# Kernel tuning notes

Measured on AMD Instinct MI355X. Metric: run time of the kernel, lower is better.

The kernel has to match this reference:

```python
import jax, jax.numpy as jnp
import numpy as np

B, S, D, H = 1, 2048, 2048, 32
HD = D // H
SCALE = float(HD) ** -0.5


def _rope(x, cos, sin):
    # x: (b, s, h, hd); interleaved-pair RoPE as in executorch apply_rotary_emb
    xr, xi = x[..., 0::2], x[..., 1::2]
    c = cos[None, :, None, :]
    s = sin[None, :, None, :]
    out = jnp.stack([xr * c - xi * s, xr * s + xi * c], axis=-1)
    return out.reshape(x.shape)


def setup_inputs() -> dict:
    key = jax.random.key(0)
    ks = jax.random.split(key, 8)
    hidden_states = jax.random.normal(ks[0], (B, S, D), jnp.float32)
    pos = jnp.arange(S, dtype=jnp.float32)
    inv = 1.0 / (10000.0 ** (jnp.arange(0, HD, 2, dtype=jnp.float32) / HD))
    ang = pos[:, None] * inv[None, :]  # (S, HD//2)
    freqs_cos = jnp.cos(ang)
    freqs_sin = jnp.sin(ang)
    causal = jnp.tril(jnp.ones((S, S), dtype=bool))
    attention_mask = jnp.where(causal, 0.0, -1e9).astype(jnp.float32)[None, None]
    k_cache = jax.random.normal(ks[1], (B, S, H, HD), jnp.float32)
    v_cache = jax.random.normal(ks[2], (B, S, H, HD), jnp.float32)
    k_mask = jnp.ones((B, S, 1, 1), jnp.float32)
    v_mask = jnp.ones((B, S, 1, 1), jnp.float32)
    # weights stored as (in, out); math-equivalent to torch Linear(out,in) @ W.T
    wq = jax.random.normal(ks[3], (D, D), jnp.float32) * 0.02
    wk = jax.random.normal(ks[4], (D, D), jnp.float32) * 0.02
    wv = jax.random.normal(ks[5], (D, D), jnp.float32) * 0.02
    wo = jax.random.normal(ks[6], (D, D), jnp.float32) * 0.02
    return {"hidden_states": hidden_states, "freqs_cos": freqs_cos,
            "freqs_sin": freqs_sin, "attention_mask": attention_mask,
            "k_cache": k_cache, "v_cache": v_cache,
            "k_mask": k_mask, "v_mask": v_mask,
            "wq": wq, "wk": wk, "wv": wv, "wo": wo}


def reference(hidden_states, freqs_cos, freqs_sin, attention_mask,
              k_cache, v_cache, k_mask, v_mask, wq, wk, wv, wo):
    b, s, _ = hidden_states.shape
    q = (hidden_states @ wq).reshape(b, s, H, HD)
    k = (hidden_states @ wk).reshape(b, s, H, HD)
    v = (hidden_states @ wv).reshape(b, s, H, HD)
    q = _rope(q, freqs_cos, freqs_sin)
    k = _rope(k, freqs_cos, freqs_sin)
    # mask-blend KV cache update
    k = k_cache * (1.0 - k_mask) + k * k_mask  # (b, S, H, HD)
    v = v_cache * (1.0 - v_mask) + v * v_mask
    qt = q.transpose(0, 2, 1, 3)  # (b, H, s, HD)
    kt = k.transpose(0, 2, 1, 3)
    vt = v.transpose(0, 2, 1, 3)
    attn = jnp.einsum('bhqd,bhkd->bhqk', qt, kt) * SCALE + attention_mask
    attn = jax.nn.softmax(attn, axis=-1)
    y = jnp.einsum('bhqk,bhkd->bhqd', attn, vt)  # (b, H, s, HD)
    # torch: y.transpose(0,1).contiguous().view(b, s, dim); valid since b == 1
    y = jnp.swapaxes(y, 0, 1).reshape(b, s, D)
    y = y @ wo
    return (y, k, v)
```

## Files before the change

kernel.cpp:

```cpp
#include <hip/hip_runtime.h>
#include <hip/hip_bf16.h>
#include <stdint.h>

typedef __bf16 bf16;
typedef __attribute__((ext_vector_type(8))) __bf16 bf16x8;
typedef __attribute__((ext_vector_type(4))) float f32x4;

#define SEQ 2048
#define DIM 2048
#define NHEAD 32
#define HD 64
#define SCALE_L2E 0.18033688011112042f

__device__ __forceinline__ void gload16(void* lds, const void* g) {
  __builtin_amdgcn_global_load_lds(
      (const __attribute__((address_space(1))) unsigned int*)g,
      (__attribute__((address_space(3))) unsigned int*)lds, 16, 0, 0);
}

__device__ __forceinline__ f32x4 mfma16(bf16x8 a, bf16x8 b, f32x4 c) {
  return __builtin_amdgcn_mfma_f32_16x16x32_bf16(a, b, c, 0, 0, 0);
}

__global__ __launch_bounds__(256) void prep(
    const float* __restrict__ hs, bf16* __restrict__ hsb,
    const float* __restrict__ w0, const float* __restrict__ w1,
    const float* __restrict__ w2, const float* __restrict__ w3,
    bf16* __restrict__ t0, bf16* __restrict__ t1,
    bf16* __restrict__ t2, bf16* __restrict__ t3) {
  int t = threadIdx.x;
  if (blockIdx.z == 4) {
    size_t i = ((size_t)(blockIdx.y * 32 + blockIdx.x) * 256 + t) * 16;
#pragma unroll
    for (int half = 0; half < 2; ++half) {
      f32x4 a = *(const f32x4*)(hs + i + half * 8);
      f32x4 b = *(const f32x4*)(hs + i + half * 8 + 4);
      bf16x8 o;
#pragma unroll
      for (int j = 0; j < 4; ++j) { o[j] = (bf16)a[j]; o[j + 4] = (bf16)b[j]; }
      *(bf16x8*)(hsb + i + half * 8) = o;
    }
    return;
  }
  const float* wsrc[4] = {w0, w1, w2, w3};
  bf16* wdst[4] = {t0, t1, t2, t3};
  const float* w = wsrc[blockIdx.z];
  bf16* wT = wdst[blockIdx.z];
  __shared__ alignas(16) bf16 tile[64][72];
  int n0 = blockIdx.x * 64, k0 = blockIdx.y * 64;
#pragma unroll
  for (int i = 0; i < 4; ++i) {
    int r = (t >> 4) + 16 * i;
    int c = (t & 15) * 4;
    f32x4 v = *(const f32x4*)(w + (size_t)(k0 + r) * DIM + n0 + c);
#pragma unroll
    for (int j = 0; j < 4; ++j) tile[r][c + j] = (bf16)v[j];
  }
  __syncthreads();
#pragma unroll
  for (int i = 0; i < 2; ++i) {
    int n = (t >> 3) + 32 * i;
    int kb = (t & 7) * 8;
    bf16x8 o;
#pragma unroll
    for (int j = 0; j < 8; ++j) o[j] = tile[kb + j][n];
    *(bf16x8*)(wT + (size_t)(n0 + n) * DIM + k0 + kb) = o;
  }
}

template <typename OutT>
__global__ __launch_bounds__(256) void gemm128(
    const bf16* __restrict__ A,
    const bf16* __restrict__ B0, const bf16* __restrict__ B1, const bf16* __restrict__ B2,
    OutT* __restrict__ C0, OutT* __restrict__ C1, OutT* __restrict__ C2,
    int M, int N, int K) {
  const bf16* Bt; OutT* C;
  if (blockIdx.z == 0)      { Bt = B0; C = C0; }
  else if (blockIdx.z == 1) { Bt = B1; C = C1; }
  else                      { Bt = B2; C = C2; }
  __shared__ alignas(16) bf16 As[128][64];
  __shared__ alignas(16) bf16 Bs[128][64];
  int tid = threadIdx.x, lane = tid & 63, w = tid >> 6;
  int wr = w >> 1, wc = w & 1;
  size_t mBase = (size_t)blockIdx.y * 128, nBase = (size_t)blockIdx.x * 128;
  f32x4 acc[4][4] = {};
  int r0 = tid >> 3, sl = tid & 7;
  int lr = lane & 15, hi = lane >> 4, sw = lr & 7;
  for (int kt = 0; kt < K; kt += 64) {
#pragma unroll
    for (int i = 0; i < 4; ++i) {
      int row = r0 + 32 * i;
      int kc = sl ^ (row & 7);
      gload16(&As[row][sl * 8], A + (mBase + row) * K + kt + kc * 8);
      gload16(&Bs[row][sl * 8], Bt + (nBase + row) * K + kt + kc * 8);
    }
    __syncthreads();
#pragma unroll
    for (int kk = 0; kk < 2; ++kk) {
      int cb = kk * 4 + hi;
      bf16x8 a[4], b[4];
#pragma unroll
      for (int m = 0; m < 4; ++m)
        a[m] = *(const bf16x8*)&As[wr * 64 + m * 16 + lr][(cb ^ sw) * 8];
#pragma unroll
      for (int n = 0; n < 4; ++n)
        b[n] = *(const bf16x8*)&Bs[wc * 64 + n * 16 + lr][(cb ^ sw) * 8];
#pragma unroll
      for (int m = 0; m < 4; ++m)
#pragma unroll
        for (int n = 0; n < 4; ++n)
          acc[m][n] = mfma16(a[m], b[n], acc[m][n]);
    }
    __syncthreads();
  }
#pragma unroll
  for (int m = 0; m < 4; ++m)
#pragma unroll
    for (int n = 0; n < 4; ++n)
#pragma unroll
      for (int j = 0; j < 4; ++j) {
        size_t row = mBase + wr * 64 + m * 16 + hi * 4 + j;
        size_t col = nBase + wc * 64 + n * 16 + lr;
        C[row * N + col] = (OutT)acc[m][n][j];
      }
}

__global__ __launch_bounds__(512) void gemm_out(
    const bf16* __restrict__ A, const bf16* __restrict__ Bt,
    float* __restrict__ Y) {
  const int K = DIM, N = DIM;
  __shared__ alignas(16) bf16 As[2][128][64];
  __shared__ alignas(16) bf16 Bs[2][128][64];
  __shared__ alignas(16) float red[128][132];
  int tid = threadIdx.x;
  int grp = tid >> 8;
  int gt = tid & 255;
  int lane = gt & 63, w = gt >> 6;
  int wr = w >> 1, wc = w & 1;
  size_t mBase = (size_t)blockIdx.y * 128, nBase = (size_t)blockIdx.x * 128;
  f32x4 acc[4][4] = {};
  int r0 = gt >> 3, sl = gt & 7;
  int lr = lane & 15, hi = lane >> 4, sw = lr & 7;
  int kbeg = grp * (K / 2);
  for (int kt = kbeg; kt < kbeg + K / 2; kt += 64) {
#pragma unroll
    for (int i = 0; i < 4; ++i) {
      int row = r0 + 32 * i;
      int kc = sl ^ (row & 7);
      gload16(&As[grp][row][sl * 8], A + (mBase + row) * K + kt + kc * 8);
      gload16(&Bs[grp][row][sl * 8], Bt + (nBase + row) * K + kt + kc * 8);
    }
    __syncthreads();
#pragma unroll
    for (int kk = 0; kk < 2; ++kk) {
      int cb = kk * 4 + hi;
      bf16x8 a[4], b[4];
#pragma unroll
      for (int m = 0; m < 4; ++m)
        a[m] = *(const bf16x8*)&As[grp][wr * 64 + m * 16 + lr][(cb ^ sw) * 8];
#pragma unroll
      for (int n = 0; n < 4; ++n)
        b[n] = *(const bf16x8*)&Bs[grp][wc * 64 + n * 16 + lr][(cb ^ sw) * 8];
#pragma unroll
      for (int m = 0; m < 4; ++m)
#pragma unroll
        for (int n = 0; n < 4; ++n)
          acc[m][n] = mfma16(a[m], b[n], acc[m][n]);
    }
    __syncthreads();
  }
  if (grp == 1) {
#pragma unroll
    for (int m = 0; m < 4; ++m)
#pragma unroll
      for (int n = 0; n < 4; ++n)
#pragma unroll
        for (int j = 0; j < 4; ++j)
          red[wr * 64 + m * 16 + hi * 4 + j][wc * 64 + n * 16 + lr] = acc[m][n][j];
  }
  __syncthreads();
  if (grp == 0) {
#pragma unroll
    for (int m = 0; m < 4; ++m)
#pragma unroll
      for (int n = 0; n < 4; ++n)
#pragma unroll
        for (int j = 0; j < 4; ++j) {
          int row = wr * 64 + m * 16 + hi * 4 + j;
          int col = wc * 64 + n * 16 + lr;
          Y[(mBase + row) * N + nBase + col] = acc[m][n][j] + red[row][col];
        }
  }
}

__global__ __launch_bounds__(256) void qkvprep(
    const bf16* __restrict__ qraw, const bf16* __restrict__ kraw,
    const bf16* __restrict__ vraw,
    const float* __restrict__ fc, const float* __restrict__ fs,
    const float* __restrict__ kcache, const float* __restrict__ kmask,
    const float* __restrict__ vcache, const float* __restrict__ vmask,
    float* __restrict__ kout, float* __restrict__ vout,
    bf16* __restrict__ qb, bf16* __restrict__ kb, bf16* __restrict__ vtb) {
  __shared__ alignas(16) bf16 tile[64][72];
  int bid = blockIdx.x;
  if (bid < SEQ) {
    int s = bid;
    int c0 = threadIdx.x * 8;
    int h = c0 >> 6, d0 = c0 & 63;
    float km = kmask[s], omk = 1.0f - km;
    size_t src = (size_t)s * DIM + c0;
    f32x4 cc = *(const f32x4*)(fc + s * 32 + (d0 >> 1));
    f32x4 ss = *(const f32x4*)(fs + s * 32 + (d0 >> 1));
    bf16x8 qv = *(const bf16x8*)(qraw + src);
    bf16x8 kv = *(const bf16x8*)(kraw + src);
    float kcf[8];
    *(f32x4*)(kcf) = *(const f32x4*)(kcache + src);
    *(f32x4*)(kcf + 4) = *(const f32x4*)(kcache + src + 4);
    bf16x8 qo, ko;
    float kof[8];
#pragma unroll
    for (int i = 0; i < 4; ++i) {
      float c = cc[i], sn = ss[i];
      float qr = (float)qv[2 * i], qi = (float)qv[2 * i + 1];
      qo[2 * i]     = (bf16)(qr * c - qi * sn);
      qo[2 * i + 1] = (bf16)(qr * sn + qi * c);
      float kr = (float)kv[2 * i], ki = (float)kv[2 * i + 1];
      float b0 = kcf[2 * i] * omk + (kr * c - ki * sn) * km;
      float b1 = kcf[2 * i + 1] * omk + (kr * sn + ki * c) * km;
      kof[2 * i] = b0; kof[2 * i + 1] = b1;
      ko[2 * i] = (bf16)b0; ko[2 * i + 1] = (bf16)b1;
    }
    *(f32x4*)(kout + src) = *(f32x4*)kof;
    *(f32x4*)(kout + src + 4) = *(f32x4*)(kof + 4);
    size_t dsth = ((size_t)h * SEQ + s) * HD + d0;
    *(bf16x8*)(qb + dsth) = qo;
    *(bf16x8*)(kb + dsth) = ko;
    return;
  }
  int vb = bid - SEQ;
  int h = vb >> 5;
  int s0 = (vb & 31) * 64;
  int t = threadIdx.x;
#pragma unroll
  for (int i = 0; i < 4; ++i) {
    int r = (t >> 4) + 16 * i;
    int c = (t & 15) * 4;
    int s = s0 + r;
    float vm = vmask[s], om = 1.0f - vm;
    size_t src = (size_t)s * DIM + h * 64 + c;
    f32x4 vc = *(const f32x4*)(vcache + src);
    f32x4 o;
#pragma unroll
    for (int j = 0; j < 4; ++j) {
      float val = vc[j] * om + (float)vraw[src + j] * vm;
      o[j] = val;
      tile[r][c + j] = (bf16)val;
    }
    *(f32x4*)(vout + src) = o;
  }
  __syncthreads();
#pragma unroll
  for (int i = 0; i < 2; ++i) {
    int hd = (t >> 3) + 32 * i;
    int cb = (t & 7) * 8;
    bf16x8 o;
#pragma unroll
    for (int j = 0; j < 8; ++j) o[j] = tile[cb + j][hd];
    *(bf16x8*)(vtb + (size_t)h * HD * SEQ + (size_t)hd * SEQ + s0 + cb) = o;
  }
}

__global__ __launch_bounds__(512) void attn_fwd(
    const bf16* __restrict__ qb, const bf16* __restrict__ kb,
    const bf16* __restrict__ vtb, bf16* __restrict__ ob) {
  int orig = blockIdx.x;
  int wg = (orig & 7) * 32 + (orig >> 3);
  int h = wg >> 3;
  int qp = wg & 7;
  int qtA = qp, qtB = 15 - qp;
  int ntA = qtA + 1;
  const int NT = 17;
  __shared__ alignas(16) bf16 Ks[2][128][64];
  __shared__ alignas(16) bf16 Vs[2][64][128];
  __shared__ alignas(16) bf16 Ps[8][16][128];
  int tid = threadIdx.x, lane = tid & 63, w = tid >> 6;
  const bf16* qh = qb + (size_t)h * SEQ * HD;
  const bf16* kh = kb + (size_t)h * SEQ * HD;
  const bf16* vh = vtb + (size_t)h * HD * SEQ;
  int lr = lane & 15, hi = lane >> 4, sw = lr & 7;
  int qrowA = qtA * 128 + w * 16 + lr;
  int qrowB = qtB * 128 + w * 16 + lr;
  bf16x8 qfA[2], qfB[2];
#pragma unroll
  for (int kk = 0; kk < 2; ++kk) {
    qfA[kk] = *(const bf16x8*)(qh + (size_t)qrowA * HD + kk * 32 + hi * 8);
    qfB[kk] = *(const bf16x8*)(qh + (size_t)qrowB * HD + kk * 32 + hi * 8);
  }
  f32x4 otA[4] = {}, otB[4] = {};
  float mA = -3e38f, lA = 0.f, mB = -3e38f, lB = 0.f;
  char* PsW = (char*)&Ps[w][0][0];

  auto STAGE = [&](int kv0, int b) {
    int kr0 = tid >> 3, ksl = tid & 7;
#pragma unroll
    for (int i = 0; i < 2; ++i) {
      int row = kr0 + 64 * i;
      int kc = ksl ^ (row & 7);
      gload16(&Ks[b][row][ksl * 8], kh + (size_t)(kv0 + row) * HD + kc * 8);
    }
    int vr0 = tid >> 4, vsl = tid & 15;
#pragma unroll
    for (int i = 0; i < 2; ++i) {
      int row = vr0 + 32 * i;
      int vc = vsl ^ (row & 7);
      gload16(&Vs[b][row][vsl * 8], vh + (size_t)row * SEQ + kv0 + vc * 8);
    }
  };

  auto BODY = [&](int buf, int kv0, bf16x8 (&qf)[2], f32x4 (&ot)[4],
                  float& mrun, float& lrun, int qrow, bool last) {
    f32x4 st[8] = {};
    __builtin_amdgcn_s_setprio(1);
#pragma unroll
    for (int kk = 0; kk < 2; ++kk) {
      int cb = kk * 4 + hi;
#pragma unroll
      for (int n = 0; n < 8; ++n) {
        bf16x8 kf = *(const bf16x8*)&Ks[buf][n * 16 + lr][(cb ^ sw) * 8];
        st[n] = mfma16(kf, qf[kk], st[n]);
      }
    }
    __builtin_amdgcn_s_setprio(0);
    if (last) {
#pragma unroll
      for (int n = 0; n < 8; ++n)
#pragma unroll
        for (int j = 0; j < 4; ++j) {
          int key = kv0 + n * 16 + hi * 4 + j;
          st[n][j] = (key <= qrow) ? st[n][j] * SCALE_L2E : -1e30f;
        }
    } else {
#pragma unroll
      for (int n = 0; n < 8; ++n)
#pragma unroll
        for (int j = 0; j < 4; ++j) st[n][j] *= SCALE_L2E;
    }
    float tm[8];
#pragma unroll
    for (int n = 0; n < 8; ++n)
      tm[n] = fmaxf(fmaxf(st[n][0], st[n][1]), fmaxf(st[n][2], st[n][3]));
    float t01 = fmaxf(tm[0], tm[1]), t23 = fmaxf(tm[2], tm[3]);
    float t45 = fmaxf(tm[4], tm[5]), t67 = fmaxf(tm[6], tm[7]);
    float tmax = fmaxf(fmaxf(t01, t23), fmaxf(t45, t67));
    tmax = fmaxf(tmax, __shfl_xor(tmax, 16));
    tmax = fmaxf(tmax, __shfl_xor(tmax, 32));
    if (!__all(tmax <= mrun + 8.f)) {
      float mnew = fmaxf(mrun, tmax);
      float alpha = exp2f(mrun - mnew);
      mrun = mnew;
      lrun *= alpha;
#pragma unroll
      for (int nd = 0; nd < 4; ++nd)
#pragma unroll
        for (int j = 0; j < 4; ++j) ot[nd][j] *= alpha;
    }
    float ps[8];
#pragma unroll
    for (int n = 0; n < 8; ++n) {
      float p0 = exp2f(st[n][0] - mrun), p1 = exp2f(st[n][1] - mrun);
      float p2 = exp2f(st[n][2] - mrun), p3 = exp2f(st[n][3] - mrun);
      st[n][0] = p0; st[n][1] = p1; st[n][2] = p2; st[n][3] = p3;
      ps[n] = (p0 + p1) + (p2 + p3);
    }
    float psum = ((ps[0] + ps[1]) + (ps[2] + ps[3])) +
                 ((ps[4] + ps[5]) + (ps[6] + ps[7]));
    psum += __shfl_xor(psum, 16);
    psum += __shfl_xor(psum, 32);
    lrun += psum;
#pragma unroll
    for (int n = 0; n < 8; ++n) {
      union { bf16 b[4]; uint2 u; } pk;
#pragma unroll
      for (int j = 0; j < 4; ++j) pk.b[j] = (bf16)st[n][j];
      int keyc = n * 2 + (hi >> 1);
      *(uint2*)(PsW + lr * 256 + ((keyc ^ sw) * 16) + (hi & 1) * 8) = pk.u;
    }
    __builtin_amdgcn_s_setprio(1);
#pragma unroll
    for (int kk = 0; kk < 4; ++kk) {
      int cb = kk * 4 + hi;
      bf16x8 pf = *(const bf16x8*)(PsW + lr * 256 + ((cb ^ sw) * 16));
#pragma unroll
      for (int nd = 0; nd < 4; ++nd) {
        bf16x8 vf = *(const bf16x8*)&Vs[buf][nd * 16 + lr][(cb ^ sw) * 8];
        ot[nd] = mfma16(vf, pf, ot[nd]);
      }
    }
    __builtin_amdgcn_s_setprio(0);
  };

  auto STORE = [&](f32x4 (&ot)[4], float lrun, int qrow) {
    float rinv = 1.0f / lrun;
    bf16* orow = ob + ((size_t)h * SEQ + qrow) * HD;
#pragma unroll
    for (int nd = 0; nd < 4; ++nd) {
      union { bf16 b[4]; uint2 u; } o;
#pragma unroll
      for (int j = 0; j < 4; ++j) o.b[j] = (bf16)(ot[nd][j] * rinv);
      *(uint2*)(orow + nd * 16 + hi * 4) = o.u;
    }
  };

  STAGE(0, 0);
  int buf = 0;
  for (int t = 0; t < NT; ++t) {
    __syncthreads();
    if (t + 1 < NT) {
      int tn = t + 1;
      int kvn = (tn < ntA ? tn : tn - ntA) * 128;
      STAGE(kvn, buf ^ 1);
    }
    if (t < ntA) {
      int kv0 = t * 128;
      BODY(buf, kv0, qfA, otA, mA, lA, qrowA, t == ntA - 1);
      if (t == ntA - 1) STORE(otA, lA, qrowA);
    } else {
      int kv0 = (t - ntA) * 128;
      BODY(buf, kv0, qfB, otB, mB, lB, qrowB, t == NT - 1);
    }
    buf ^= 1;
  }
  STORE(otB, lB, qrowB);
}

extern "C" void kernel_launch(void* const* d_in, const int* in_sizes, int n_in,
                              void* d_out, int out_size, void* d_ws, size_t ws_size,
                              hipStream_t stream) {
  const float* hs     = (const float*)d_in[0];
  const float* fc     = (const float*)d_in[1];
  const float* fs     = (const float*)d_in[2];
  const float* kcache = (const float*)d_in[4];
  const float* vcache = (const float*)d_in[5];
  const float* kmask  = (const float*)d_in[6];
  const float* vmask  = (const float*)d_in[7];
  const float* wq     = (const float*)d_in[8];
  const float* wk     = (const float*)d_in[9];
  const float* wv     = (const float*)d_in[10];
  const float* wo     = (const float*)d_in[11];

  float* y    = (float*)d_out;
  float* kout = y + (size_t)SEQ * DIM;
  float* vout = y + 2 * (size_t)SEQ * DIM;

  char* ws = (char*)d_ws;
  const size_t MB8 = (size_t)SEQ * DIM * sizeof(bf16);
  bf16* wqT  = (bf16*)(ws + 0 * MB8);
  bf16* wkT  = (bf16*)(ws + 1 * MB8);
  bf16* wvT  = (bf16*)(ws + 2 * MB8);
  bf16* woT  = (bf16*)(ws + 3 * MB8);
  bf16* hsb  = (bf16*)(ws + 4 * MB8);
  bf16* qraw = (bf16*)(ws + 5 * MB8);
  bf16* kraw = (bf16*)(ws + 6 * MB8);
  bf16* vraw = (bf16*)(ws + 7 * MB8);
  bf16* qb   = (bf16*)(ws + 8 * MB8);
  bf16* kb   = (bf16*)(ws + 9 * MB8);
  bf16* vtb  = (bf16*)(ws + 10 * MB8);
  bf16* ob   = hsb;

  prep<<<dim3(32, 32, 5), dim3(256), 0, stream>>>(
      hs, hsb, wq, wk, wv, wo, wqT, wkT, wvT, woT);
  gemm128<bf16><<<dim3(16, 16, 3), dim3(256), 0, stream>>>(
      hsb, wqT, wkT, wvT, qraw, kraw, vraw, SEQ, DIM, DIM);
  qkvprep<<<dim3(SEQ + 1024), dim3(256), 0, stream>>>(
      qraw, kraw, vraw, fc, fs, kcache, kmask, vcache, vmask,
      kout, vout, qb, kb, vtb);
  attn_fwd<<<dim3(256), dim3(512), 0, stream>>>(qb, kb, vtb, ob);
  gemm_out<<<dim3(16, 16), dim3(512), 0, stream>>>(ob, woT, y);
}
```

Baseline: 188.0 us.

## Replace QKV projection GEMM with 256x256 tiled, double-buffered 8-wave pipelined kernel

Replaces the single-buffered 128x128 QKV GEMM with a 256x256 tile kernel using 512 threads (8 waves), double-buffered LDS split into two k-halves, and prefetch of upcoming k-slices interleaved with MFMA phases under barriers and setprio. It also remaps blocks with a swizzled tile order and uses a new LDS XOR swizzle. The aims are to overlap global loads with compute, raise arithmetic intensity per tile, and cut sync stalls. The cost is higher register pressure (8x4 accumulators) and fewer blocks (192) spread across the CUs.

```diff
diff --git a/kernel.cpp b/kernel.cpp
--- a/kernel.cpp
+++ b/kernel.cpp
@@ -68,60 +68,93 @@
   }
 }
 
-template <typename OutT>
-__global__ __launch_bounds__(256) void gemm128(
+__global__ __launch_bounds__(512, 2) void gemm8p(
     const bf16* __restrict__ A,
     const bf16* __restrict__ B0, const bf16* __restrict__ B1, const bf16* __restrict__ B2,
-    OutT* __restrict__ C0, OutT* __restrict__ C1, OutT* __restrict__ C2,
-    int M, int N, int K) {
-  const bf16* Bt; OutT* C;
+    bf16* __restrict__ C0, bf16* __restrict__ C1, bf16* __restrict__ C2) {
+  const int K = DIM, N = DIM;
+  const bf16* Bt; bf16* C;
   if (blockIdx.z == 0)      { Bt = B0; C = C0; }
   else if (blockIdx.z == 1) { Bt = B1; C = C1; }
   else                      { Bt = B2; C = C2; }
-  __shared__ alignas(16) bf16 As[128][64];
-  __shared__ alignas(16) bf16 Bs[128][64];
-  int tid = threadIdx.x, lane = tid & 63, w = tid >> 6;
-  int wr = w >> 1, wc = w & 1;
-  size_t mBase = (size_t)blockIdx.y * 128, nBase = (size_t)blockIdx.x * 128;
-  f32x4 acc[4][4] = {};
-  int r0 = tid >> 3, sl = tid & 7;
-  int lr = lane & 15, hi = lane >> 4, sw = lr & 7;
-  for (int kt = 0; kt < K; kt += 64) {
-#pragma unroll
-    for (int i = 0; i < 4; ++i) {
-      int row = r0 + 32 * i;
-      int kc = sl ^ (row & 7);
-      gload16(&As[row][sl * 8], A + (mBase + row) * K + kt + kc * 8);
-      gload16(&Bs[row][sl * 8], Bt + (nBase + row) * K + kt + kc * 8);
-    }
-    __syncthreads();
-#pragma unroll
-    for (int kk = 0; kk < 2; ++kk) {
-      int cb = kk * 4 + hi;
-      bf16x8 a[4], b[4];
-#pragma unroll
-      for (int m = 0; m < 4; ++m)
-        a[m] = *(const bf16x8*)&As[wr * 64 + m * 16 + lr][(cb ^ sw) * 8];
-#pragma unroll
-      for (int n = 0; n < 4; ++n)
-        b[n] = *(const bf16x8*)&Bs[wc * 64 + n * 16 + lr][(cb ^ sw) * 8];
-#pragma unroll
-      for (int m = 0; m < 4; ++m)
+  __shared__ alignas(16) bf16 As[2][2][256][32];
+  __shared__ alignas(16) bf16 Bs[2][2][256][32];
+  int o = blockIdx.y * 8 + blockIdx.x;
+  int wgs = (o & 7) * 8 + (o >> 3);
+  size_t mBase = (size_t)(wgs >> 3) * 256;
+  size_t nBase = (size_t)(wgs & 7) * 256;
+  int tid = threadIdx.x, lane = tid & 63, wid = tid >> 6;
+  int wr = wid >> 2, wc = wid & 3;
+  int lr = lane & 15, hi = lane >> 4;
+  f32x4 acc[8][4] = {};
+
+  auto STG = [&](const bf16* src, bf16 (*dst)[2][256][32], int T, int s,
+                 int b, size_t rbase) {
+#pragma unroll
+    for (int i = 0; i < 2; ++i) {
+      int oo = i * 512 + tid;
+      int row = oo >> 2;
+      int cp = oo & 3;
+      int cl = cp ^ ((row >> 1) & 3);
+      gload16(&dst[b][s][row][cp * 8],
+              src + (rbase + row) * K + T * 64 + s * 32 + cl * 8);
+    }
+  };
+
+  STG(A, As, 0, 0, 0, mBase); STG(Bt, Bs, 0, 0, 0, nBase);
+  STG(A, As, 0, 1, 0, mBase); STG(Bt, Bs, 0, 1, 0, nBase);
+  STG(A, As, 1, 0, 1, mBase); STG(Bt, Bs, 1, 0, 1, nBase);
+  asm volatile("s_waitcnt vmcnt(8)" ::: "memory");
+  __builtin_amdgcn_s_barrier();
+
+  bf16x8 bsr[4];
+  for (int T = 0; T < 32; ++T) {
+    int cur = T & 1;
+#pragma unroll
+    for (int q = 0; q < 4; ++q) {
+      const int s = q >> 1, f = q & 1;
+      bf16x8 ar[4];
+#pragma unroll
+      for (int mm = 0; mm < 4; ++mm) {
+        int row = wr * 128 + (f * 4 + mm) * 16 + lr;
+        int cp = hi ^ ((row >> 1) & 3);
+        ar[mm] = *(const bf16x8*)&As[cur][s][row][cp * 8];
+      }
+      if (f == 0) {
+#pragma unroll
+        for (int n = 0; n < 4; ++n) {
+          int row = wc * 64 + n * 16 + lr;
+          int cp = hi ^ ((row >> 1) & 3);
+          bsr[n] = *(const bf16x8*)&Bs[cur][s][row][cp * 8];
+        }
+      }
+      if (q == 0) { if (T + 1 < 32) STG(A,  As, T + 1, 1, cur ^ 1, mBase); }
+      else if (q == 1) { if (T + 1 < 32) STG(Bt, Bs, T + 1, 1, cur ^ 1, nBase); }
+      else if (q == 2) { if (T + 2 < 32) STG(A,  As, T + 2, 0, cur, mBase); }
+      else             { if (T + 2 < 32) STG(Bt, Bs, T + 2, 0, cur, nBase); }
+      __builtin_amdgcn_s_barrier();
+      asm volatile("s_waitcnt lgkmcnt(0)");
+      __builtin_amdgcn_sched_barrier(0);
+      __builtin_amdgcn_s_setprio(1);
+#pragma unroll
+      for (int mm = 0; mm < 4; ++mm)
 #pragma unroll
         for (int n = 0; n < 4; ++n)
-          acc[m][n] = mfma16(a[m], b[n], acc[m][n]);
-    }
-    __syncthreads();
-  }
-#pragma unroll
-  for (int m = 0; m < 4; ++m)
+          acc[f * 4 + mm][n] = mfma16(ar[mm], bsr[n], acc[f * 4 + mm][n]);
+      __builtin_amdgcn_s_setprio(0);
+      if (q & 1) asm volatile("s_waitcnt vmcnt(8)" ::: "memory");
+      __builtin_amdgcn_s_barrier();
+    }
+  }
+#pragma unroll
+  for (int m = 0; m < 8; ++m)
 #pragma unroll
     for (int n = 0; n < 4; ++n)
 #pragma unroll
       for (int j = 0; j < 4; ++j) {
-        size_t row = mBase + wr * 64 + m * 16 + hi * 4 + j;
+        size_t row = mBase + wr * 128 + m * 16 + hi * 4 + j;
         size_t col = nBase + wc * 64 + n * 16 + lr;
-        C[row * N + col] = (OutT)acc[m][n][j];
+        C[row * N + col] = (bf16)acc[m][n][j];
       }
 }
 
@@ -469,8 +502,8 @@
 
   prep<<<dim3(32, 32, 5), dim3(256), 0, stream>>>(
       hs, hsb, wq, wk, wv, wo, wqT, wkT, wvT, woT);
-  gemm128<bf16><<<dim3(16, 16, 3), dim3(256), 0, stream>>>(
-      hsb, wqT, wkT, wvT, qraw, kraw, vraw, SEQ, DIM, DIM);
+  gemm8p<<<dim3(8, 8, 3), dim3(512), 0, stream>>>(
+      hsb, wqT, wkT, wvT, qraw, kraw, vraw);
   qkvprep<<<dim3(SEQ + 1024), dim3(256), 0, stream>>>(
       qraw, kraw, vraw, fc, fs, kcache, kmask, vcache, vmask,
       kout, vout, qb, kb, vtb);
```

Measured after the change: 206.4 us. 9.8% more time.
